# Kernel optimization log

Hardware: AMD Instinct MI355X
Metric: run time of the kernel (lower is better)

The kernel has to match this reference:

```python
import jax, jax.numpy as jnp
import numpy as np

EPS = 1e-5
GROUPS = 8


def _bn(x, gamma, beta, mean, var, axis):
    # inference-mode batchnorm along `axis`
    shape = [1] * x.ndim
    shape[axis] = -1
    scale = gamma.reshape(shape) * jax.lax.rsqrt(var.reshape(shape) + EPS)
    return (x - mean.reshape(shape)) * scale + beta.reshape(shape)


def setup_inputs() -> dict:
    key = jax.random.key(0)
    ks = jax.random.split(key, 16)
    N, C, H, W = 8, 128, 128, 128
    out_planes = 128
    x = jax.random.normal(ks[0], (N, C, H, W), jnp.float32)
    w_qkv = jax.random.normal(ks[1], (2 * out_planes, C), jnp.float32) * np.float32(np.sqrt(1.0 / C))

    def bn_params(k, c):
        k1, k2, k3, k4 = jax.random.split(k, 4)
        gamma = jax.random.uniform(k1, (c,), jnp.float32, 0.5, 1.5)
        beta = jax.random.normal(k2, (c,), jnp.float32) * 0.1
        mean = jax.random.normal(k3, (c,), jnp.float32) * 0.1
        var = jax.random.uniform(k4, (c,), jnp.float32, 0.5, 1.5)
        return gamma, beta, mean, var

    qg, qb, qm, qv = bn_params(ks[2], 2 * out_planes)
    sg, sb, sm, sv = bn_params(ks[3], GROUPS)
    og, ob, om, ov = bn_params(ks[4], out_planes)
    return {
        'x': x, 'w_qkv': w_qkv,
        'qkv_gamma': qg, 'qkv_beta': qb, 'qkv_mean': qm, 'qkv_var': qv,
        'sim_gamma': sg, 'sim_beta': sb, 'sim_mean': sm, 'sim_var': sv,
        'out_gamma': og, 'out_beta': ob, 'out_mean': om, 'out_var': ov,
    }


def reference(x, w_qkv, qkv_gamma, qkv_beta, qkv_mean, qkv_var,
              sim_gamma, sim_beta, sim_mean, sim_var,
              out_gamma, out_beta, out_mean, out_var):
    N, C, H, W = x.shape
    groups = GROUPS
    out_planes = w_qkv.shape[0] // 2
    gp = out_planes // groups  # group_planes

    # width=False: (N,C,H,W) -> (N,W,C,H) -> (N*W, C, H)
    xb = jnp.transpose(x, (0, 3, 1, 2)).reshape(N * W, C, H)
    # conv1x1 qkv transform + BN1d over channels
    qkv = jnp.einsum('bci,oc->boi', xb, w_qkv)
    qkv = _bn(qkv, qkv_gamma, qkv_beta, qkv_mean, qkv_var, axis=1)
    qkv = qkv.reshape(N * W, groups, 2 * gp, H)
    q = qkv[:, :, : gp // 2]          # (NW, g, gp/2, H)
    k = qkv[:, :, gp // 2: gp]        # (NW, g, gp/2, H)
    v = qkv[:, :, gp:]                # (NW, g, gp,   H)

    qk = jnp.einsum('bgci,bgcj->bgij', q, k)  # (NW, g, H, H)
    sim = _bn(qk, sim_gamma, sim_beta, sim_mean, sim_var, axis=1)
    sim = jax.nn.softmax(sim, axis=3)

    sv = jnp.einsum('bgij,bgcj->bgci', sim, v)  # (NW, g, gp, H)
    sv = sv.reshape(N * W, out_planes, H)
    out = _bn(sv, out_gamma, out_beta, out_mean, out_var, axis=1)
    out = out.reshape(N, W, out_planes, H)
    # permute(0,2,3,1): (N, out_planes, H, W)
    return jnp.transpose(out, (0, 2, 3, 1))
```

## Files before the change

### kernel.cpp

```cpp
#include <hip/hip_runtime.h>
#include <math.h>

#define EPS 1e-5f

typedef _Float16 half4 __attribute__((ext_vector_type(4)));
typedef _Float16 half8 __attribute__((ext_vector_type(8)));
typedef float floatx4 __attribute__((ext_vector_type(4)));

__global__ void transpose_cvt_k(const float* __restrict__ x, _Float16* __restrict__ xt2) {
  __shared__ float tile[64][65];
  int nh = blockIdx.x;
  int n = nh >> 7, h = nh & 127;
  int c0 = blockIdx.y * 64, w0 = blockIdx.z * 64;
  const float* src = x + (size_t)n * 2097152 + (size_t)h * 128;
  _Float16* dst = xt2 + (size_t)n * 2097152 + (size_t)h * 128;
  int lane = threadIdx.x & 63;
  int tr = threadIdx.x >> 6;
#pragma unroll
  for (int rr = tr; rr < 64; rr += 4)
    tile[rr][lane] = src[(size_t)(c0 + rr) * 16384 + w0 + lane];
  __syncthreads();
#pragma unroll
  for (int cc = tr; cc < 64; cc += 4)
    dst[(size_t)(w0 + cc) * 16384 + c0 + lane] = (_Float16)tile[lane][cc];
}

__global__ void __launch_bounds__(256, 2) qkv_mfma_kernel(
    const _Float16* __restrict__ xt2, const float* __restrict__ wq,
    const float* __restrict__ qg, const float* __restrict__ qb,
    const float* __restrict__ qm, const float* __restrict__ qv,
    _Float16* __restrict__ qkv16) {
  __shared__ _Float16 As[128][136];
  __shared__ _Float16 Bs[128][136];
  __shared__ float scs[128];
  __shared__ float bis[128];
  int b = blockIdx.x >> 1;
  int oh = blockIdx.x & 1;
  int t = threadIdx.x;

  {
    const float* wbase = wq + (size_t)oh * 128 * 128;
#pragma unroll
    for (int idx = t; idx < 4096; idx += 256) {
      int o = idx >> 5, c4 = (idx & 31) * 4;
      float4 v = *(const float4*)(wbase + (size_t)o * 128 + c4);
      As[o][c4 + 0] = (_Float16)v.x;
      As[o][c4 + 1] = (_Float16)v.y;
      As[o][c4 + 2] = (_Float16)v.z;
      As[o][c4 + 3] = (_Float16)v.w;
    }
  }
  {
    const _Float16* xb = xt2 + (size_t)b * 16384;
#pragma unroll
    for (int idx = t; idx < 2048; idx += 256) {
      int i = idx >> 4, c8 = (idx & 15) * 8;
      half8 v = *(const half8*)(xb + (size_t)i * 128 + c8);
      *(half8*)(&Bs[i][c8]) = v;
    }
  }
  if (t < 128) {
    int o = oh * 128 + t;
    float sc = qg[o] * rsqrtf(qv[o] + EPS);
    scs[t] = sc;
    bis[t] = qb[o] - qm[o] * sc;
  }
  __syncthreads();

  int wv = t >> 6;
  int lane = t & 63;
  int m0 = (wv & 1) * 64;
  int n0 = (wv >> 1) * 64;
  int lrow = lane & 15;
  int quad = lane >> 4;

  floatx4 acc[4][4];
#pragma unroll
  for (int mt = 0; mt < 4; mt++)
#pragma unroll
    for (int nt = 0; nt < 4; nt++)
#pragma unroll
      for (int r = 0; r < 4; r++) acc[mt][nt][r] = 0.f;

#pragma unroll
  for (int k0 = 0; k0 < 128; k0 += 32) {
    half8 af[4], bf[4];
#pragma unroll
    for (int mt = 0; mt < 4; mt++)
      af[mt] = *(const half8*)(&As[m0 + mt * 16 + lrow][k0 + quad * 8]);
#pragma unroll
    for (int nt = 0; nt < 4; nt++)
      bf[nt] = *(const half8*)(&Bs[n0 + nt * 16 + lrow][k0 + quad * 8]);
#pragma unroll
    for (int mt = 0; mt < 4; mt++)
#pragma unroll
      for (int nt = 0; nt < 4; nt++)
        acc[mt][nt] = __builtin_amdgcn_mfma_f32_16x16x32_f16(af[mt], bf[nt], acc[mt][nt], 0, 0, 0);
  }

  _Float16* outb = qkv16 + (size_t)b * 32768 + (size_t)oh * 16384;
#pragma unroll
  for (int mt = 0; mt < 4; mt++) {
#pragma unroll
    for (int r = 0; r < 4; r++) {
      int o_l = m0 + mt * 16 + quad * 4 + r;
      float sc = scs[o_l];
      float bi = bis[o_l];
#pragma unroll
      for (int nt = 0; nt < 4; nt++) {
        int i = n0 + nt * 16 + lrow;
        outb[(size_t)o_l * 128 + i] = (_Float16)fmaf(acc[mt][nt][r], sc, bi);
      }
    }
  }
}

__global__ void __launch_bounds__(64) attn_mfma_kernel(
    const _Float16* __restrict__ qkv16,
    const float* __restrict__ sg, const float* __restrict__ sb,
    const float* __restrict__ sm, const float* __restrict__ svv,
    const float* __restrict__ og, const float* __restrict__ ob,
    const float* __restrict__ om, const float* __restrict__ ov,
    _Float16* __restrict__ svout) {
  __shared__ _Float16 plds[16 * 136];
  int bg = blockIdx.x;
  int b = bg >> 3, g = bg & 7;
  int t = threadIdx.x;
  int n = t & 15;
  int q4 = t >> 4;

  const _Float16* base = qkv16 + (size_t)b * 32768 + (size_t)g * 4096;
  const _Float16* kb = base + 1024;
  const _Float16* vb = base + 2048;

  half8 kf[8];
#pragma unroll
  for (int jt = 0; jt < 8; jt++)
#pragma unroll
    for (int jj = 0; jj < 8; jj++)
      kf[jt][jj] = kb[jj * 128 + jt * 16 + n];

  half8 vf[4];
#pragma unroll
  for (int ks = 0; ks < 4; ks++)
    vf[ks] = *(const half8*)(vb + (size_t)n * 128 + ks * 32 + q4 * 8);

  float s_scale = sg[g] * rsqrtf(svv[g] + EPS);
  float sc4 = s_scale * 0.25f;
  float s_bias = sb[g] - sm[g] * s_scale;

  float osc[4], obi[4];
#pragma unroll
  for (int r = 0; r < 4; r++) {
    int oc = g * 16 + q4 * 4 + r;
    float s0 = og[oc] * rsqrtf(ov[oc] + EPS);
    osc[r] = s0;
    obi[r] = ob[oc] - om[oc] * s0;
  }

  for (int st8 = 0; st8 < 8; st8++) {
    half8 qf;
#pragma unroll
    for (int jj = 0; jj < 8; jj++)
      qf[jj] = base[jj * 128 + st8 * 16 + n];

    floatx4 stt[8];
#pragma unroll
    for (int jt = 0; jt < 8; jt++) {
      floatx4 z = {0.f, 0.f, 0.f, 0.f};
      stt[jt] = __builtin_amdgcn_mfma_f32_16x16x32_f16(kf[jt], qf, z, 0, 0, 0);
    }

    float mx = -1e30f;
#pragma unroll
    for (int jt = 0; jt < 8; jt++)
#pragma unroll
      for (int r = 0; r < 4; r++) {
        stt[jt][r] = fmaf(stt[jt][r], sc4, s_bias);
        mx = fmaxf(mx, stt[jt][r]);
      }
    mx = fmaxf(mx, __shfl_xor(mx, 16));
    mx = fmaxf(mx, __shfl_xor(mx, 32));

    float ls = 0.f;
#pragma unroll
    for (int jt = 0; jt < 8; jt++)
#pragma unroll
      for (int r = 0; r < 4; r++) {
        float e = __expf(stt[jt][r] - mx);
        stt[jt][r] = e;
        ls += e;
      }
    ls += __shfl_xor(ls, 16);
    ls += __shfl_xor(ls, 32);

#pragma unroll
    for (int jt = 0; jt < 8; jt++) {
      half4 h;
      h[0] = (_Float16)stt[jt][0];
      h[1] = (_Float16)stt[jt][1];
      h[2] = (_Float16)stt[jt][2];
      h[3] = (_Float16)stt[jt][3];
      *(half4*)(&plds[n * 136 + jt * 16 + q4 * 4]) = h;
    }

    floatx4 oacc = {0.f, 0.f, 0.f, 0.f};
#pragma unroll
    for (int ks = 0; ks < 4; ks++) {
      half8 pf = *(const half8*)(&plds[n * 136 + ks * 32 + q4 * 8]);
      oacc = __builtin_amdgcn_mfma_f32_16x16x32_f16(vf[ks], pf, oacc, 0, 0, 0);
    }

    float invl = 1.f / ls;
    _Float16* outp = svout + ((size_t)b * 128 + g * 16 + q4 * 4) * 128 + st8 * 16 + n;
#pragma unroll
    for (int r = 0; r < 4; r++)
      outp[(size_t)r * 128] = (_Float16)fmaf(oacc[r] * invl, osc[r], obi[r]);
  }
}

__global__ void transpose_h2f_k(const _Float16* __restrict__ in, float* __restrict__ out,
                                int R, int C) {
  __shared__ float tile[64][65];
  int nblk = blockIdx.x;
  int r0 = blockIdx.y * 64;
  int c0 = blockIdx.z * 64;
  const _Float16* src = in + (size_t)nblk * R * C;
  float* dst = out + (size_t)nblk * R * C;
  int lane = threadIdx.x & 63;
  int tr = threadIdx.x >> 6;
#pragma unroll
  for (int rr = tr; rr < 64; rr += 4)
    tile[rr][lane] = (float)src[(size_t)(r0 + rr) * C + c0 + lane];
  __syncthreads();
#pragma unroll
  for (int cc = tr; cc < 64; cc += 4)
    dst[(size_t)(c0 + cc) * R + r0 + lane] = tile[lane][cc];
}

extern "C" void kernel_launch(void* const* d_in, const int* in_sizes, int n_in,
                              void* d_out, int out_size, void* d_ws, size_t ws_size,
                              hipStream_t stream) {
  const float* x  = (const float*)d_in[0];
  const float* wq = (const float*)d_in[1];
  const float* qg = (const float*)d_in[2];
  const float* qb = (const float*)d_in[3];
  const float* qm = (const float*)d_in[4];
  const float* qv = (const float*)d_in[5];
  const float* sg = (const float*)d_in[6];
  const float* sb = (const float*)d_in[7];
  const float* sm = (const float*)d_in[8];
  const float* sv = (const float*)d_in[9];
  const float* og = (const float*)d_in[10];
  const float* ob = (const float*)d_in[11];
  const float* om = (const float*)d_in[12];
  const float* ov = (const float*)d_in[13];
  float* out = (float*)d_out;

  _Float16* qkv16 = (_Float16*)d_ws;
  _Float16* xt2 = qkv16 + (size_t)1024 * 256 * 128;
  _Float16* svh = xt2 + (size_t)1024 * 128 * 128;

  transpose_cvt_k<<<dim3(1024, 2, 2), 256, 0, stream>>>(x, xt2);
  qkv_mfma_kernel<<<2048, 256, 0, stream>>>(xt2, wq, qg, qb, qm, qv, qkv16);
  attn_mfma_kernel<<<8192, 64, 0, stream>>>(qkv16, sg, sb, sm, sv, og, ob, om, ov, svh);
  transpose_h2f_k<<<dim3(8, 2, 256), 256, 0, stream>>>(svh, out, 128, 16384);
}
```

Measured before the change: 262.2 us.

## Fuse QKV projection GEMM with attention per two-group slice in LDS

Merges the qkv projection kernel and the attention kernel into one single-wave kernel. Each block computes the 64 qkv output channels for two groups of one batch-column, applies BN, and keeps them in LDS for the attention step. This removes the fp16 qkv workspace round trip through global memory and one kernel launch. In exchange, each block reads the x slice and weights straight from global memory without LDS sharing, the x slice is re-read by four blocks, and the 128 accumulator registers per lane may cost occupancy.

```diff
diff --git a/kernel.cpp b/kernel.cpp
--- a/kernel.cpp
+++ b/kernel.cpp
@@ -25,197 +25,167 @@
     dst[(size_t)(w0 + cc) * 16384 + c0 + lane] = (_Float16)tile[lane][cc];
 }
 
-__global__ void __launch_bounds__(256, 2) qkv_mfma_kernel(
+__global__ void __launch_bounds__(64, 2) fused_qkv_attn(
     const _Float16* __restrict__ xt2, const float* __restrict__ wq,
     const float* __restrict__ qg, const float* __restrict__ qb,
     const float* __restrict__ qm, const float* __restrict__ qv,
-    _Float16* __restrict__ qkv16) {
-  __shared__ _Float16 As[128][136];
-  __shared__ _Float16 Bs[128][136];
-  __shared__ float scs[128];
-  __shared__ float bis[128];
-  int b = blockIdx.x >> 1;
-  int oh = blockIdx.x & 1;
-  int t = threadIdx.x;
-
-  {
-    const float* wbase = wq + (size_t)oh * 128 * 128;
-#pragma unroll
-    for (int idx = t; idx < 4096; idx += 256) {
-      int o = idx >> 5, c4 = (idx & 31) * 4;
-      float4 v = *(const float4*)(wbase + (size_t)o * 128 + c4);
-      As[o][c4 + 0] = (_Float16)v.x;
-      As[o][c4 + 1] = (_Float16)v.y;
-      As[o][c4 + 2] = (_Float16)v.z;
-      As[o][c4 + 3] = (_Float16)v.w;
-    }
-  }
-  {
-    const _Float16* xb = xt2 + (size_t)b * 16384;
-#pragma unroll
-    for (int idx = t; idx < 2048; idx += 256) {
-      int i = idx >> 4, c8 = (idx & 15) * 8;
-      half8 v = *(const half8*)(xb + (size_t)i * 128 + c8);
-      *(half8*)(&Bs[i][c8]) = v;
-    }
-  }
-  if (t < 128) {
-    int o = oh * 128 + t;
-    float sc = qg[o] * rsqrtf(qv[o] + EPS);
-    scs[t] = sc;
-    bis[t] = qb[o] - qm[o] * sc;
-  }
-  __syncthreads();
-
-  int wv = t >> 6;
-  int lane = t & 63;
-  int m0 = (wv & 1) * 64;
-  int n0 = (wv >> 1) * 64;
-  int lrow = lane & 15;
-  int quad = lane >> 4;
-
-  floatx4 acc[4][4];
-#pragma unroll
-  for (int mt = 0; mt < 4; mt++)
-#pragma unroll
-    for (int nt = 0; nt < 4; nt++)
-#pragma unroll
-      for (int r = 0; r < 4; r++) acc[mt][nt][r] = 0.f;
-
-#pragma unroll
-  for (int k0 = 0; k0 < 128; k0 += 32) {
-    half8 af[4], bf[4];
-#pragma unroll
-    for (int mt = 0; mt < 4; mt++)
-      af[mt] = *(const half8*)(&As[m0 + mt * 16 + lrow][k0 + quad * 8]);
-#pragma unroll
-    for (int nt = 0; nt < 4; nt++)
-      bf[nt] = *(const half8*)(&Bs[n0 + nt * 16 + lrow][k0 + quad * 8]);
-#pragma unroll
-    for (int mt = 0; mt < 4; mt++)
-#pragma unroll
-      for (int nt = 0; nt < 4; nt++)
-        acc[mt][nt] = __builtin_amdgcn_mfma_f32_16x16x32_f16(af[mt], bf[nt], acc[mt][nt], 0, 0, 0);
-  }
-
-  _Float16* outb = qkv16 + (size_t)b * 32768 + (size_t)oh * 16384;
-#pragma unroll
-  for (int mt = 0; mt < 4; mt++) {
-#pragma unroll
-    for (int r = 0; r < 4; r++) {
-      int o_l = m0 + mt * 16 + quad * 4 + r;
-      float sc = scs[o_l];
-      float bi = bis[o_l];
-#pragma unroll
-      for (int nt = 0; nt < 4; nt++) {
-        int i = n0 + nt * 16 + lrow;
-        outb[(size_t)o_l * 128 + i] = (_Float16)fmaf(acc[mt][nt][r], sc, bi);
-      }
-    }
-  }
-}
-
-__global__ void __launch_bounds__(64) attn_mfma_kernel(
-    const _Float16* __restrict__ qkv16,
     const float* __restrict__ sg, const float* __restrict__ sb,
     const float* __restrict__ sm, const float* __restrict__ svv,
     const float* __restrict__ og, const float* __restrict__ ob,
     const float* __restrict__ om, const float* __restrict__ ov,
     _Float16* __restrict__ svout) {
+  __shared__ _Float16 qkvlds[128 * 72];
   __shared__ _Float16 plds[16 * 136];
-  int bg = blockIdx.x;
-  int b = bg >> 3, g = bg & 7;
+  int bq = blockIdx.x;
+  int b = bq & 1023;
+  int qtr = bq >> 10;
   int t = threadIdx.x;
   int n = t & 15;
   int q4 = t >> 4;
 
-  const _Float16* base = qkv16 + (size_t)b * 32768 + (size_t)g * 4096;
-  const _Float16* kb = base + 1024;
-  const _Float16* vb = base + 2048;
-
-  half8 kf[8];
-#pragma unroll
-  for (int jt = 0; jt < 8; jt++)
-#pragma unroll
-    for (int jj = 0; jj < 8; jj++)
-      kf[jt][jj] = kb[jj * 128 + jt * 16 + n];
-
-  half8 vf[4];
-#pragma unroll
-  for (int ks = 0; ks < 4; ks++)
-    vf[ks] = *(const half8*)(vb + (size_t)n * 128 + ks * 32 + q4 * 8);
-
-  float s_scale = sg[g] * rsqrtf(svv[g] + EPS);
-  float sc4 = s_scale * 0.25f;
-  float s_bias = sb[g] - sm[g] * s_scale;
-
-  float osc[4], obi[4];
-#pragma unroll
-  for (int r = 0; r < 4; r++) {
-    int oc = g * 16 + q4 * 4 + r;
-    float s0 = og[oc] * rsqrtf(ov[oc] + EPS);
-    osc[r] = s0;
-    obi[r] = ob[oc] - om[oc] * s0;
+  const _Float16* xb = xt2 + (size_t)b * 16384;
+
+  floatx4 acc[4][8];
+#pragma unroll
+  for (int mt = 0; mt < 4; mt++)
+#pragma unroll
+    for (int nt = 0; nt < 8; nt++)
+#pragma unroll
+      for (int r = 0; r < 4; r++) acc[mt][nt][r] = 0.f;
+
+#pragma unroll
+  for (int k0 = 0; k0 < 128; k0 += 32) {
+    half8 af[4];
+#pragma unroll
+    for (int mt = 0; mt < 4; mt++) {
+      const float* wp = wq + (size_t)(qtr * 64 + mt * 16 + n) * 128 + k0 + q4 * 8;
+      float4 a0 = *(const float4*)wp;
+      float4 a1 = *(const float4*)(wp + 4);
+      half8 h;
+      h[0] = (_Float16)a0.x; h[1] = (_Float16)a0.y; h[2] = (_Float16)a0.z; h[3] = (_Float16)a0.w;
+      h[4] = (_Float16)a1.x; h[5] = (_Float16)a1.y; h[6] = (_Float16)a1.z; h[7] = (_Float16)a1.w;
+      af[mt] = h;
+    }
+    half8 bf[8];
+#pragma unroll
+    for (int nt = 0; nt < 8; nt++)
+      bf[nt] = *(const half8*)(xb + (size_t)(nt * 16 + n) * 128 + k0 + q4 * 8);
+#pragma unroll
+    for (int mt = 0; mt < 4; mt++)
+#pragma unroll
+      for (int nt = 0; nt < 8; nt++)
+        acc[mt][nt] = __builtin_amdgcn_mfma_f32_16x16x32_f16(af[mt], bf[nt], acc[mt][nt], 0, 0, 0);
   }
 
-  for (int st8 = 0; st8 < 8; st8++) {
-    half8 qf;
-#pragma unroll
-    for (int jj = 0; jj < 8; jj++)
-      qf[jj] = base[jj * 128 + st8 * 16 + n];
-
-    floatx4 stt[8];
-#pragma unroll
-    for (int jt = 0; jt < 8; jt++) {
-      floatx4 z = {0.f, 0.f, 0.f, 0.f};
-      stt[jt] = __builtin_amdgcn_mfma_f32_16x16x32_f16(kf[jt], qf, z, 0, 0, 0);
-    }
-
-    float mx = -1e30f;
+  float qsc[4][4], qbi[4][4];
+#pragma unroll
+  for (int mt = 0; mt < 4; mt++)
+#pragma unroll
+    for (int r = 0; r < 4; r++) {
+      int o = qtr * 64 + mt * 16 + q4 * 4 + r;
+      float sc = qg[o] * rsqrtf(qv[o] + EPS);
+      qsc[mt][r] = sc;
+      qbi[mt][r] = qb[o] - qm[o] * sc;
+    }
+
+#pragma unroll
+  for (int mt = 0; mt < 4; mt++)
+#pragma unroll
+    for (int nt = 0; nt < 8; nt++) {
+      int h = nt * 16 + n;
+      half4 hh;
+#pragma unroll
+      for (int r = 0; r < 4; r++)
+        hh[r] = (_Float16)fmaf(acc[mt][nt][r], qsc[mt][r], qbi[mt][r]);
+      *(half4*)(&qkvlds[h * 72 + mt * 16 + q4 * 4]) = hh;
+    }
+
+#pragma unroll 1
+  for (int gl = 0; gl < 2; gl++) {
+    int g = qtr * 2 + gl;
+    int chb = gl * 32;
+
+    half8 kf[8];
 #pragma unroll
     for (int jt = 0; jt < 8; jt++)
-#pragma unroll
-      for (int r = 0; r < 4; r++) {
-        stt[jt][r] = fmaf(stt[jt][r], sc4, s_bias);
-        mx = fmaxf(mx, stt[jt][r]);
+      kf[jt] = *(const half8*)(&qkvlds[(jt * 16 + n) * 72 + chb + 8]);
+
+    half8 vf[4];
+#pragma unroll
+    for (int ks = 0; ks < 4; ks++)
+#pragma unroll
+      for (int jj = 0; jj < 8; jj++)
+        vf[ks][jj] = qkvlds[(ks * 32 + q4 * 8 + jj) * 72 + chb + 16 + n];
+
+    float s_scale = sg[g] * rsqrtf(svv[g] + EPS);
+    float sc4 = s_scale * 0.25f;
+    float s_bias = sb[g] - sm[g] * s_scale;
+
+    float osc[4], obi[4];
+#pragma unroll
+    for (int r = 0; r < 4; r++) {
+      int oc = g * 16 + q4 * 4 + r;
+      float s0 = og[oc] * rsqrtf(ov[oc] + EPS);
+      osc[r] = s0;
+      obi[r] = ob[oc] - om[oc] * s0;
+    }
+
+    for (int st8 = 0; st8 < 8; st8++) {
+      half8 qf = *(const half8*)(&qkvlds[(st8 * 16 + n) * 72 + chb]);
+
+      floatx4 stt[8];
+#pragma unroll
+      for (int jt = 0; jt < 8; jt++) {
+        floatx4 z = {0.f, 0.f, 0.f, 0.f};
+        stt[jt] = __builtin_amdgcn_mfma_f32_16x16x32_f16(kf[jt], qf, z, 0, 0, 0);
       }
-    mx = fmaxf(mx, __shfl_xor(mx, 16));
-    mx = fmaxf(mx, __shfl_xor(mx, 32));
-
-    float ls = 0.f;
-#pragma unroll
-    for (int jt = 0; jt < 8; jt++)
-#pragma unroll
-      for (int r = 0; r < 4; r++) {
-        float e = __expf(stt[jt][r] - mx);
-        stt[jt][r] = e;
-        ls += e;
+
+      float mx = -1e30f;
+#pragma unroll
+      for (int jt = 0; jt < 8; jt++)
+#pragma unroll
+        for (int r = 0; r < 4; r++) {
+          stt[jt][r] = fmaf(stt[jt][r], sc4, s_bias);
+          mx = fmaxf(mx, stt[jt][r]);
+        }
+      mx = fmaxf(mx, __shfl_xor(mx, 16));
+      mx = fmaxf(mx, __shfl_xor(mx, 32));
+
+      float ls = 0.f;
+#pragma unroll
+      for (int jt = 0; jt < 8; jt++)
+#pragma unroll
+        for (int r = 0; r < 4; r++) {
+          float e = __expf(stt[jt][r] - mx);
+          stt[jt][r] = e;
+          ls += e;
+        }
+      ls += __shfl_xor(ls, 16);
+      ls += __shfl_xor(ls, 32);
+
+#pragma unroll
+      for (int jt = 0; jt < 8; jt++) {
+        half4 h;
+        h[0] = (_Float16)stt[jt][0];
+        h[1] = (_Float16)stt[jt][1];
+        h[2] = (_Float16)stt[jt][2];
+        h[3] = (_Float16)stt[jt][3];
+        *(half4*)(&plds[n * 136 + jt * 16 + q4 * 4]) = h;
       }
-    ls += __shfl_xor(ls, 16);
-    ls += __shfl_xor(ls, 32);
-
-#pragma unroll
-    for (int jt = 0; jt < 8; jt++) {
-      half4 h;
-      h[0] = (_Float16)stt[jt][0];
-      h[1] = (_Float16)stt[jt][1];
-      h[2] = (_Float16)stt[jt][2];
-      h[3] = (_Float16)stt[jt][3];
-      *(half4*)(&plds[n * 136 + jt * 16 + q4 * 4]) = h;
-    }
-
-    floatx4 oacc = {0.f, 0.f, 0.f, 0.f};
-#pragma unroll
-    for (int ks = 0; ks < 4; ks++) {
-      half8 pf = *(const half8*)(&plds[n * 136 + ks * 32 + q4 * 8]);
-      oacc = __builtin_amdgcn_mfma_f32_16x16x32_f16(vf[ks], pf, oacc, 0, 0, 0);
-    }
-
-    float invl = 1.f / ls;
-    _Float16* outp = svout + ((size_t)b * 128 + g * 16 + q4 * 4) * 128 + st8 * 16 + n;
-#pragma unroll
-    for (int r = 0; r < 4; r++)
-      outp[(size_t)r * 128] = (_Float16)fmaf(oacc[r] * invl, osc[r], obi[r]);
+
+      floatx4 oacc = {0.f, 0.f, 0.f, 0.f};
+#pragma unroll
+      for (int ks = 0; ks < 4; ks++) {
+        half8 pf = *(const half8*)(&plds[n * 136 + ks * 32 + q4 * 8]);
+        oacc = __builtin_amdgcn_mfma_f32_16x16x32_f16(vf[ks], pf, oacc, 0, 0, 0);
+      }
+
+      float invl = 1.f / ls;
+      _Float16* outp = svout + ((size_t)b * 128 + g * 16 + q4 * 4) * 128 + st8 * 16 + n;
+#pragma unroll
+      for (int r = 0; r < 4; r++)
+        outp[(size_t)r * 128] = (_Float16)fmaf(oacc[r] * invl, osc[r], obi[r]);
+    }
   }
 }
 
@@ -257,12 +227,11 @@
   const float* ov = (const float*)d_in[13];
   float* out = (float*)d_out;
 
-  _Float16* qkv16 = (_Float16*)d_ws;
-  _Float16* xt2 = qkv16 + (size_t)1024 * 256 * 128;
+  _Float16* xt2 = (_Float16*)d_ws;
   _Float16* svh = xt2 + (size_t)1024 * 128 * 128;
 
   transpose_cvt_k<<<dim3(1024, 2, 2), 256, 0, stream>>>(x, xt2);
-  qkv_mfma_kernel<<<2048, 256, 0, stream>>>(xt2, wq, qg, qb, qm, qv, qkv16);
-  attn_mfma_kernel<<<8192, 64, 0, stream>>>(qkv16, sg, sb, sm, sv, og, ob, om, ov, svh);
+  fused_qkv_attn<<<4096, 64, 0, stream>>>(xt2, wq, qg, qb, qm, qv,
+                                          sg, sb, sm, sv, og, ob, om, ov, svh);
   transpose_h2f_k<<<dim3(8, 2, 256), 256, 0, stream>>>(svh, out, 128, 16384);
 }
```

After: 265.1 us. Within noise of the previous version (+1.1%).
